# Performance work log

Measured on AMD Instinct MI355X. Metric: run time of the kernel, lower is better.

The kernel has to match this reference:

```python
import jax, jax.numpy as jnp
import numpy as np

B, S, A, C, E, H = 256, 512, 8, 256, 64, 256

def _lin_params(key, din, dout):
    k1, k2 = jax.random.split(key)
    bound = 1.0 / np.sqrt(din)
    w = jax.random.uniform(k1, (din, dout), minval=-bound, maxval=bound, dtype=jnp.float32)
    b = jax.random.uniform(k2, (dout,), minval=-bound, maxval=bound, dtype=jnp.float32)
    return w, b

def setup_inputs() -> dict:
    key = jax.random.key(0)
    ks = jax.random.split(key, 9)
    q = jax.random.normal(ks[0], (B, S, A), dtype=jnp.float32)
    st = jax.random.normal(ks[1], (B, S, C), dtype=jnp.float32)
    w1a, b1a = _lin_params(ks[2], C, H)
    w1b, b1b = _lin_params(ks[3], H, A * E)
    w2a, b2a = _lin_params(ks[4], C, H)
    w2b, b2b = _lin_params(ks[5], H, E)
    wb1, bb1 = _lin_params(ks[6], C, E)
    wb2a, bb2a = _lin_params(ks[7], C, H)
    wb2b, bb2b = _lin_params(ks[8], H, 1)
    return dict(agent_q_values=q, central_states=st,
                w1a=w1a, b1a=b1a, w1b=w1b, b1b=b1b,
                w2a=w2a, b2a=b2a, w2b=w2b, b2b=b2b,
                wb1=wb1, bb1=bb1,
                wb2a=wb2a, bb2a=bb2a, wb2b=wb2b, bb2b=bb2b)

def _mlp(x, wa, ba, wb, bb):
    # Linear -> ELU -> Linear
    h = jax.nn.elu(x @ wa + ba)
    return h @ wb + bb

def reference(agent_q_values, central_states,
              w1a, b1a, w1b, b1b,
              w2a, b2a, w2b, b2b,
              wb1, bb1,
              wb2a, bb2a, wb2b, bb2b):
    bsz, seq, na = agent_q_values.shape
    st = central_states.reshape(-1, C)                      # [N, C]
    q = agent_q_values.reshape(-1, na)                      # [N, A]
    w1 = jnp.abs(_mlp(st, w1a, b1a, w1b, b1b)).reshape(-1, na, E)   # [N, A, E]
    b1 = st @ wb1 + bb1                                     # [N, E]
    w2 = jnp.abs(_mlp(st, w2a, b2a, w2b, b2b))              # [N, E]
    b2 = _mlp(st, wb2a, bb2a, wb2b, bb2b)                   # [N, 1]
    hidden = jax.nn.relu(jnp.einsum('na,nae->ne', q, w1) + b1)      # [N, E]
    joint = jnp.einsum('ne,ne->n', hidden, w2)[:, None] + b2        # [N, 1]
    return joint.reshape(bsz, seq, 1)
```

## Files before the change

kernel.cpp:

```cpp
#include <hip/hip_runtime.h>
#include <math.h>

typedef __bf16 bf16_t;
typedef bf16_t bf16x8 __attribute__((ext_vector_type(8)));
typedef float  floatx4 __attribute__((ext_vector_type(4)));

#define MFMA16(a, b, c) __builtin_amdgcn_mfma_f32_16x16x32_bf16((a), (b), (c), 0, 0, 0)

constexpr int NTOT = 256 * 512;
constexpr int CDIM = 256;

constexpr int N_TILES  = 88;
constexpr int WS_ELEMS = N_TILES * 4096;

__global__ void prep_weights(const float* __restrict__ w1a, const float* __restrict__ w1b,
                             const float* __restrict__ w2a, const float* __restrict__ w2b,
                             const float* __restrict__ wb1, const float* __restrict__ wb2a,
                             bf16_t* __restrict__ ws) {
  int idx = blockIdx.x * 256 + threadIdx.x;
  if (idx >= WS_ELEMS) return;
  int t   = idx >> 12;
  int rel = idx & 4095;
  const float* src; int dout; int ct;
  if      (t < 16) { src = w1a;  dout = 256; ct = t; }
  else if (t < 20) { src = wb1;  dout = 64;  ct = t - 16; }
  else if (t < 52) { src = w1b;  dout = 512; ct = t - 20; }
  else if (t < 68) { src = w2a;  dout = 256; ct = t - 52; }
  else if (t < 72) { src = w2b;  dout = 64;  ct = t - 68; }
  else             { src = wb2a; dout = 256; ct = t - 72; }
  int j    = rel & 7;
  int lane = (rel >> 3) & 63;
  int ks   = rel >> 9;
  int o = ct * 16 + (lane & 15);
  int k = ks * 32 + (lane >> 4) * 8 + j;
  ws[idx] = (bf16_t)src[(size_t)k * dout + o];
}

__device__ __forceinline__ void gload_lds16(const bf16_t* g, bf16_t* l) {
  __builtin_amdgcn_global_load_lds(
      (const __attribute__((address_space(1))) unsigned int*)g,
      (__attribute__((address_space(3))) unsigned int*)l, 16, 0, 0);
}

__global__ __launch_bounds__(256, 3)
void mixing_fused(const float* __restrict__ q,
                  const float* __restrict__ st,
                  const bf16_t* __restrict__ W,
                  const float* __restrict__ b1a, const float* __restrict__ b1b,
                  const float* __restrict__ b2a, const float* __restrict__ b2b,
                  const float* __restrict__ bb1,
                  const float* __restrict__ bb2a,
                  const float* __restrict__ wb2b, const float* __restrict__ bb2b,
                  float* __restrict__ out) {
  __shared__ __align__(16) bf16_t wbuf[2][8192];
  __shared__ __align__(16) bf16_t t_s[4][32][36];
  __shared__ __align__(16) float  q_s[4][256];

  const int tid  = threadIdx.x;
  const int wid  = tid >> 6;
  const int lane = tid & 63;
  const int l15  = lane & 15;
  const int quad = lane >> 4;
  const int m0   = blockIdx.x * 128 + wid * 32;

  auto stage = [&](int g) {
    const bf16_t* src = W + (size_t)g * 8192 + wid * 2048 + lane * 8;
    bf16_t* dst = &wbuf[g & 1][wid * 2048];
#pragma unroll
    for (int i = 0; i < 4; ++i)
      gload_lds16(src + i * 512, dst + i * 512);
  };

  *(float4*)&q_s[wid][lane * 4] = *(const float4*)(q + (size_t)m0 * 8 + lane * 4);

  bf16x8 sA[2][8];
#pragma unroll
  for (int rt = 0; rt < 2; ++rt) {
    const float* rp = st + (size_t)(m0 + rt * 16 + l15) * CDIM;
#pragma unroll
    for (int ks = 0; ks < 8; ++ks) {
      int k0 = ks * 32 + quad * 8;
      float4 f0 = *(const float4*)(rp + k0);
      float4 f1 = *(const float4*)(rp + k0 + 4);
      bf16x8 v;
      v[0] = (bf16_t)f0.x; v[1] = (bf16_t)f0.y; v[2] = (bf16_t)f0.z; v[3] = (bf16_t)f0.w;
      v[4] = (bf16_t)f1.x; v[5] = (bf16_t)f1.y; v[6] = (bf16_t)f1.z; v[7] = (bf16_t)f1.w;
      sA[rt][ks] = v;
    }
  }

  auto gemmL = [&](int buf, int h, const bf16x8 (&A)[2][8], floatx4 (&acc)[2]) {
    floatx4 z = {0.f, 0.f, 0.f, 0.f};
    acc[0] = z; acc[1] = z;
#pragma unroll
    for (int kk = 0; kk < 8; ++kk) {
      bf16x8 b = *(const bf16x8*)&wbuf[buf][h * 4096 + kk * 512 + lane * 8];
      acc[0] = MFMA16(A[0][kk], b, acc[0]);
      acc[1] = MFMA16(A[1][kk], b, acc[1]);
    }
  };

  stage(0);

  bf16x8 hA[2][8];

#pragma unroll
  for (int ks = 0; ks < 8; ++ks) {
    __syncthreads();
    stage(ks + 1);
    const int buf = ks & 1;
#pragma unroll
    for (int h = 0; h < 2; ++h) {
      int ct = 2 * ks + h;
      floatx4 acc[2];
      gemmL(buf, h, sA, acc);
      float bias = b1a[ct * 16 + l15];
#pragma unroll
      for (int rt = 0; rt < 2; ++rt)
#pragma unroll
        for (int i = 0; i < 4; ++i) {
          float v = acc[rt][i] + bias;
          v = v > 0.f ? v : (__expf(v) - 1.f);
          t_s[wid][rt * 16 + quad * 4 + i][h * 16 + l15] = (bf16_t)v;
        }
    }
#pragma unroll
    for (int rt = 0; rt < 2; ++rt)
      hA[rt][ks] = *(const bf16x8*)&t_s[wid][rt * 16 + l15][quad * 8];
  }

  floatx4 hid[2][4];
#pragma unroll
  for (int gg = 0; gg < 2; ++gg) {
    __syncthreads();
    stage(9 + gg);
    const int buf = gg & 1;
#pragma unroll
    for (int h = 0; h < 2; ++h) {
      int et = 2 * gg + h;
      floatx4 acc[2];
      gemmL(buf, h, sA, acc);
      float bias = bb1[et * 16 + l15];
      hid[0][et] = acc[0] + bias;
      hid[1][et] = acc[1] + bias;
    }
  }

#pragma unroll 1
  for (int a = 0; a < 8; ++a) {
    float qv[2][4];
#pragma unroll
    for (int rt = 0; rt < 2; ++rt)
#pragma unroll
      for (int i = 0; i < 4; ++i)
        qv[rt][i] = q_s[wid][(rt * 16 + quad * 4 + i) * 8 + a];
#pragma unroll
    for (int g2 = 0; g2 < 2; ++g2) {
      const int idx = a * 2 + g2;
      __syncthreads();
      stage(11 + idx);
      const int buf = g2;
#pragma unroll
      for (int h = 0; h < 2; ++h) {
        int ct = a * 4 + g2 * 2 + h;
        const int et = g2 * 2 + h;
        floatx4 acc[2];
        gemmL(buf, h, hA, acc);
        float bias = b1b[ct * 16 + l15];
#pragma unroll
        for (int rt = 0; rt < 2; ++rt)
#pragma unroll
          for (int i = 0; i < 4; ++i) {
            float w1v = fabsf(acc[rt][i] + bias);
            hid[rt][et][i] += qv[rt][i] * w1v;
          }
      }
    }
  }
#pragma unroll
  for (int rt = 0; rt < 2; ++rt)
#pragma unroll
    for (int et = 0; et < 4; ++et)
#pragma unroll
      for (int i = 0; i < 4; ++i) hid[rt][et][i] = fmaxf(hid[rt][et][i], 0.f);

#pragma unroll
  for (int ks = 0; ks < 8; ++ks) {
    __syncthreads();
    stage(27 + ks);
    const int buf = ks & 1;
#pragma unroll
    for (int h = 0; h < 2; ++h) {
      int ct = 2 * ks + h;
      floatx4 acc[2];
      gemmL(buf, h, sA, acc);
      float bias = b2a[ct * 16 + l15];
#pragma unroll
      for (int rt = 0; rt < 2; ++rt)
#pragma unroll
        for (int i = 0; i < 4; ++i) {
          float v = acc[rt][i] + bias;
          v = v > 0.f ? v : (__expf(v) - 1.f);
          t_s[wid][rt * 16 + quad * 4 + i][h * 16 + l15] = (bf16_t)v;
        }
    }
#pragma unroll
    for (int rt = 0; rt < 2; ++rt)
      hA[rt][ks] = *(const bf16x8*)&t_s[wid][rt * 16 + l15][quad * 8];
  }

  float p[2][4] = {{0.f, 0.f, 0.f, 0.f}, {0.f, 0.f, 0.f, 0.f}};
#pragma unroll
  for (int gg = 0; gg < 2; ++gg) {
    __syncthreads();
    stage(35 + gg);
    const int buf = gg & 1;
#pragma unroll
    for (int h = 0; h < 2; ++h) {
      int et = 2 * gg + h;
      floatx4 acc[2];
      gemmL(buf, h, hA, acc);
      float bias = b2b[et * 16 + l15];
#pragma unroll
      for (int rt = 0; rt < 2; ++rt)
#pragma unroll
        for (int i = 0; i < 4; ++i) {
          float w2v = fabsf(acc[rt][i] + bias);
          p[rt][i] += hid[rt][et][i] * w2v;
        }
    }
  }

#pragma unroll 1
  for (int gg = 0; gg < 8; ++gg) {
    __syncthreads();
    if (gg < 7) stage(37 + gg);
    const int buf = gg & 1;
#pragma unroll
    for (int h = 0; h < 2; ++h) {
      int ct = 2 * gg + h;
      floatx4 acc[2];
      gemmL(buf, h, sA, acc);
      float bias = bb2a[ct * 16 + l15];
      float wv   = wb2b[ct * 16 + l15];
#pragma unroll
      for (int rt = 0; rt < 2; ++rt)
#pragma unroll
        for (int i = 0; i < 4; ++i) {
          float v = acc[rt][i] + bias;
          v = v > 0.f ? v : (__expf(v) - 1.f);
          p[rt][i] += v * wv;
        }
    }
  }

  float bb2 = bb2b[0];
#pragma unroll
  for (int rt = 0; rt < 2; ++rt)
#pragma unroll
    for (int i = 0; i < 4; ++i) {
      float v = p[rt][i];
      v += __shfl_xor(v, 1);
      v += __shfl_xor(v, 2);
      v += __shfl_xor(v, 4);
      v += __shfl_xor(v, 8);
      if (l15 == 0) out[m0 + rt * 16 + quad * 4 + i] = v + bb2;
    }
}

extern "C" void kernel_launch(void* const* d_in, const int* in_sizes, int n_in,
                              void* d_out, int out_size, void* d_ws, size_t ws_size,
                              hipStream_t stream) {
  const float* q    = (const float*)d_in[0];
  const float* st   = (const float*)d_in[1];
  const float* w1a  = (const float*)d_in[2];
  const float* b1a  = (const float*)d_in[3];
  const float* w1b  = (const float*)d_in[4];
  const float* b1b  = (const float*)d_in[5];
  const float* w2a  = (const float*)d_in[6];
  const float* b2a  = (const float*)d_in[7];
  const float* w2b  = (const float*)d_in[8];
  const float* b2b  = (const float*)d_in[9];
  const float* wb1  = (const float*)d_in[10];
  const float* bb1  = (const float*)d_in[11];
  const float* wb2a = (const float*)d_in[12];
  const float* bb2a = (const float*)d_in[13];
  const float* wb2b = (const float*)d_in[14];
  const float* bb2b = (const float*)d_in[15];
  bf16_t* W = (bf16_t*)d_ws;

  hipLaunchKernelGGL(prep_weights, dim3((WS_ELEMS + 255) / 256), dim3(256), 0, stream,
                     w1a, w1b, w2a, w2b, wb1, wb2a, W);
  hipLaunchKernelGGL(mixing_fused, dim3(NTOT / 128), dim3(256), 0, stream,
                     q, st, W, b1a, b1b, b2a, b2b, bb1, bb2a, wb2b, bb2b, (float*)d_out);
}
```

Before: 350.9 us.

## Reorder hypernet stages and pack live state to cut register pressure

Computes the b1 projection first, then packs the hidden accumulators into bf16 while the w1a MLP runs, and unpacks them afterwards. It also reloads the state operand sA from global memory before later stages instead of keeping it live across the whole kernel. The intent is to shrink peak VGPR usage so spills drop or occupancy rises. In exchange it adds redundant global loads and conversions of the state rows, and rounds the b1/hidden values to bf16, which loses some precision.

```diff
diff --git a/kernel.cpp b/kernel.cpp
--- a/kernel.cpp
+++ b/kernel.cpp
@@ -22,8 +22,8 @@
   int t   = idx >> 12;
   int rel = idx & 4095;
   const float* src; int dout; int ct;
-  if      (t < 16) { src = w1a;  dout = 256; ct = t; }
-  else if (t < 20) { src = wb1;  dout = 64;  ct = t - 16; }
+  if      (t < 4)  { src = wb1;  dout = 64;  ct = t; }
+  else if (t < 20) { src = w1a;  dout = 256; ct = t - 4; }
   else if (t < 52) { src = w1b;  dout = 512; ct = t - 20; }
   else if (t < 68) { src = w2a;  dout = 256; ct = t - 52; }
   else if (t < 72) { src = w2b;  dout = 64;  ct = t - 68; }
@@ -73,21 +73,22 @@
 
   *(float4*)&q_s[wid][lane * 4] = *(const float4*)(q + (size_t)m0 * 8 + lane * 4);
 
-  bf16x8 sA[2][8];
-#pragma unroll
-  for (int rt = 0; rt < 2; ++rt) {
-    const float* rp = st + (size_t)(m0 + rt * 16 + l15) * CDIM;
-#pragma unroll
-    for (int ks = 0; ks < 8; ++ks) {
-      int k0 = ks * 32 + quad * 8;
-      float4 f0 = *(const float4*)(rp + k0);
-      float4 f1 = *(const float4*)(rp + k0 + 4);
-      bf16x8 v;
-      v[0] = (bf16_t)f0.x; v[1] = (bf16_t)f0.y; v[2] = (bf16_t)f0.z; v[3] = (bf16_t)f0.w;
-      v[4] = (bf16_t)f1.x; v[5] = (bf16_t)f1.y; v[6] = (bf16_t)f1.z; v[7] = (bf16_t)f1.w;
-      sA[rt][ks] = v;
-    }
-  }
+  auto loadSA = [&](bf16x8 (&A)[2][8]) {
+#pragma unroll
+    for (int rt = 0; rt < 2; ++rt) {
+      const float* rp = st + (size_t)(m0 + rt * 16 + l15) * CDIM;
+#pragma unroll
+      for (int ks = 0; ks < 8; ++ks) {
+        int k0 = ks * 32 + quad * 8;
+        float4 f0 = *(const float4*)(rp + k0);
+        float4 f1 = *(const float4*)(rp + k0 + 4);
+        bf16x8 v;
+        v[0] = (bf16_t)f0.x; v[1] = (bf16_t)f0.y; v[2] = (bf16_t)f0.z; v[3] = (bf16_t)f0.w;
+        v[4] = (bf16_t)f1.x; v[5] = (bf16_t)f1.y; v[6] = (bf16_t)f1.z; v[7] = (bf16_t)f1.w;
+        A[rt][ks] = v;
+      }
+    }
+  };
 
   auto gemmL = [&](int buf, int h, const bf16x8 (&A)[2][8], floatx4 (&acc)[2]) {
     floatx4 z = {0.f, 0.f, 0.f, 0.f};
@@ -100,14 +101,41 @@
     }
   };
 
+  bf16x8 sA[2][8];
+  loadSA(sA);
+
   stage(0);
 
+  floatx4 hid[2][4];
+#pragma unroll
+  for (int gg = 0; gg < 2; ++gg) {
+    __syncthreads();
+    stage(1 + gg);
+    const int buf = gg & 1;
+#pragma unroll
+    for (int h = 0; h < 2; ++h) {
+      int et = 2 * gg + h;
+      floatx4 acc[2];
+      gemmL(buf, h, sA, acc);
+      float bias = bb1[et * 16 + l15];
+      hid[0][et] = acc[0] + bias;
+      hid[1][et] = acc[1] + bias;
+    }
+  }
+  bf16x8 hidp[2][2];
+#pragma unroll
+  for (int rt = 0; rt < 2; ++rt)
+#pragma unroll
+    for (int g = 0; g < 2; ++g)
+#pragma unroll
+      for (int j = 0; j < 8; ++j)
+        hidp[rt][g][j] = (bf16_t)hid[rt][g * 2 + (j >> 2)][j & 3];
+
   bf16x8 hA[2][8];
-
 #pragma unroll
   for (int ks = 0; ks < 8; ++ks) {
     __syncthreads();
-    stage(ks + 1);
+    stage(3 + ks);
     const int buf = ks & 1;
 #pragma unroll
     for (int h = 0; h < 2; ++h) {
@@ -129,22 +157,13 @@
       hA[rt][ks] = *(const bf16x8*)&t_s[wid][rt * 16 + l15][quad * 8];
   }
 
-  floatx4 hid[2][4];
-#pragma unroll
-  for (int gg = 0; gg < 2; ++gg) {
-    __syncthreads();
-    stage(9 + gg);
-    const int buf = gg & 1;
-#pragma unroll
-    for (int h = 0; h < 2; ++h) {
-      int et = 2 * gg + h;
-      floatx4 acc[2];
-      gemmL(buf, h, sA, acc);
-      float bias = bb1[et * 16 + l15];
-      hid[0][et] = acc[0] + bias;
-      hid[1][et] = acc[1] + bias;
-    }
-  }
+#pragma unroll
+  for (int rt = 0; rt < 2; ++rt)
+#pragma unroll
+    for (int g = 0; g < 2; ++g)
+#pragma unroll
+      for (int j = 0; j < 8; ++j)
+        hid[rt][g * 2 + (j >> 2)][j & 3] = (float)hidp[rt][g][j];
 
 #pragma unroll 1
   for (int a = 0; a < 8; ++a) {
@@ -180,10 +199,12 @@
 #pragma unroll
   for (int rt = 0; rt < 2; ++rt)
 #pragma unroll
-    for (int et = 0; et < 4; ++et)
-#pragma unroll
-      for (int i = 0; i < 4; ++i) hid[rt][et][i] = fmaxf(hid[rt][et][i], 0.f);
-
+    for (int g = 0; g < 2; ++g)
+#pragma unroll
+      for (int j = 0; j < 8; ++j)
+        hidp[rt][g][j] = (bf16_t)fmaxf(hid[rt][g * 2 + (j >> 2)][j & 3], 0.f);
+
+  loadSA(sA);
 #pragma unroll
   for (int ks = 0; ks < 8; ++ks) {
     __syncthreads();
@@ -209,6 +230,14 @@
       hA[rt][ks] = *(const bf16x8*)&t_s[wid][rt * 16 + l15][quad * 8];
   }
 
+#pragma unroll
+  for (int rt = 0; rt < 2; ++rt)
+#pragma unroll
+    for (int g = 0; g < 2; ++g)
+#pragma unroll
+      for (int j = 0; j < 8; ++j)
+        hid[rt][g * 2 + (j >> 2)][j & 3] = (float)hidp[rt][g][j];
+
   float p[2][4] = {{0.f, 0.f, 0.f, 0.f}, {0.f, 0.f, 0.f, 0.f}};
 #pragma unroll
   for (int gg = 0; gg < 2; ++gg) {
@@ -231,6 +260,7 @@
     }
   }
 
+  loadSA(sA);
 #pragma unroll 1
   for (int gg = 0; gg < 8; ++gg) {
     __syncthreads();
```

Result: slower. 510.8 us (+45.6%).
